# Optimization experiments

Hardware: AMD Instinct MI355X
Metric: run time of the kernel (lower is better)

Reference implementation:

```python
import jax, jax.numpy as jnp
import numpy as np

IN_FEATURES = 4096
OUT_FEATURES = 4096
K = 0.5  # keep top-k fraction of weights by |score|


def setup_inputs() -> dict:
    key = jax.random.key(0)
    kx, kw, ks = jax.random.split(key, 3)
    x = jax.random.normal(kx, (8192, IN_FEATURES), dtype=jnp.float32)
    # kaiming_normal_(mode='fan_in', nonlinearity='relu'): std = sqrt(2/fan_in)
    std = float(np.sqrt(2.0 / IN_FEATURES))
    weights = jax.random.normal(kw, (OUT_FEATURES, IN_FEATURES), dtype=jnp.float32) * std
    bias = jnp.zeros((OUT_FEATURES,), dtype=jnp.float32)
    # scores init to ones in torch, but perturb so the top-k selection is non-degenerate
    scores = jnp.ones((OUT_FEATURES, IN_FEATURES), dtype=jnp.float32) + 0.01 * jax.random.normal(ks, (OUT_FEATURES, IN_FEATURES), dtype=jnp.float32)
    return {"x": x, "weights": weights, "bias": bias, "scores": scores}


def _topk_mask(s):
    # Reproduces torch sort-based thresholding: flatten, sort ascending,
    # bottom j = int((1-K)*n) entries -> 0, remaining top entries -> 1.
    flat = s.ravel()
    n = flat.shape[0]
    j = int((1.0 - K) * n)
    order = jnp.argsort(flat)  # ascending
    keep = (jnp.arange(n) >= j).astype(s.dtype)
    mask_flat = jnp.zeros((n,), dtype=s.dtype).at[order].set(keep)
    return mask_flat.reshape(s.shape)


def reference(x, weights, bias, scores):
    s = jnp.abs(scores)
    hard = _topk_mask(s)
    # straight-through estimator: forward uses hard mask, grad passes to |scores|
    mask = s + jax.lax.stop_gradient(hard - s)
    pruned = weights * mask  # [out, in]
    return x @ pruned.T + bias  # [B, out]
```

## Files before the change

### kernel.cpp

```cpp
#include <hip/hip_runtime.h>


#define NTOT   16777216u
#define JDROP  8388608u
#define MDIM   8192
#define NDIM   4096
#define KDIM   4096

typedef __bf16 v8bf __attribute__((ext_vector_type(8)));
typedef float  v4f  __attribute__((ext_vector_type(4)));

__device__ __forceinline__ unsigned short f2bf(float f){
  unsigned u = __float_as_uint(f);
  u += 0x7fffu + ((u >> 16) & 1u);
  return (unsigned short)(u >> 16);
}

__global__ void zero_hist(unsigned* hist, unsigned* h15g){
  h15g[blockIdx.x*256 + threadIdx.x] = 0u;
  if (blockIdx.x==0) hist[threadIdx.x] = 0u;
}

__global__ __launch_bounds__(256) void hist_pass(const float* __restrict__ scores,
                                                 unsigned* __restrict__ hist,
                                                 const unsigned* __restrict__ state,
                                                 int p){
  __shared__ __align__(16) unsigned char pc[256*256];
  int tid = threadIdx.x;
  unsigned* pz = (unsigned*)pc;
  #pragma unroll
  for (int k=0;k<64;++k) pz[tid + k*256] = 0u;
  __syncthreads();
  unsigned prefix = (p>0) ? state[0] : 0u;
  const float4* s4 = (const float4*)(scores + (size_t)blockIdx.x * 16384);
  for (int it=0; it<16; ++it){
    float4 v = s4[(size_t)it*256 + tid];
    #pragma unroll
    for (int e=0;e<4;++e){
      float f = (e==0)?v.x:(e==1)?v.y:(e==2)?v.z:v.w;
      unsigned u = __float_as_uint(f) & 0x7fffffffu;
      unsigned d, ok;
      if (p==0){ d = u>>23;         ok = 1u; }
      else     { d = (u>>15)&0xffu; ok = ((u>>23)==prefix); }
      if (ok) pc[d*256 + tid]++;
    }
  }
  __syncthreads();
  unsigned b = (unsigned)tid;
  const unsigned* row = (const unsigned*)(pc + b*256);
  unsigned s = 0;
  for (int kk=0;kk<64;++kk){
    int k = (kk + tid) & 63;
    unsigned w = row[k];
    s += (w & 0xffu) + ((w>>8)&0xffu) + ((w>>16)&0xffu) + (w>>24);
  }
  if (s) atomicAdd(&hist[b], s);
}

__global__ void select_pass(unsigned* hist, unsigned* state, int p){
  int lane = threadIdx.x;
  unsigned c[4];
  #pragma unroll
  for (int k=0;k<4;++k){ c[k] = hist[lane*4+k]; hist[lane*4+k] = 0u; }
  unsigned s = c[0]+c[1]+c[2]+c[3];
  unsigned inc = s;
  #pragma unroll
  for (int d=1; d<64; d<<=1){
    unsigned t = (unsigned)__shfl_up((int)inc, d, 64);
    if (lane >= d) inc += t;
  }
  unsigned excl = inc - s;
  unsigned target = (p==0) ? JDROP : state[1];
  unsigned oldpre = (p==0) ? 0u    : state[0];
  if (target >= excl && target < excl + s){
    unsigned cum = excl, digit = 0, below = 0;
    #pragma unroll
    for (int k=0;k<4;++k){
      if (target < cum + c[k]){ digit = (unsigned)lane*4u + (unsigned)k; below = cum; break; }
      cum += c[k];
    }
    state[0] = (oldpre << 8) | digit;
    state[1] = target - below;
  }
}

__global__ __launch_bounds__(256) void hist15_pass(const float* __restrict__ scores,
                                                   const unsigned* __restrict__ state,
                                                   unsigned* __restrict__ h15g){
  __shared__ unsigned h[32768];
  int tid = threadIdx.x;
  #pragma unroll
  for (int k=0;k<128;++k) h[tid + k*256] = 0u;
  __syncthreads();
  const unsigned pre16 = state[0];
  const float4* s4 = (const float4*)(scores + (size_t)blockIdx.x * 16384);
  for (int it=0; it<16; ++it){
    float4 v = s4[(size_t)it*256 + tid];
    #pragma unroll
    for (int e=0;e<4;++e){
      float f = (e==0)?v.x:(e==1)?v.y:(e==2)?v.z:v.w;
      unsigned u = __float_as_uint(f) & 0x7fffffffu;
      if ((u>>15) == pre16) atomicAdd(&h[u & 0x7fffu], 1u);
    }
  }
  __syncthreads();
  #pragma unroll
  for (int k=0;k<128;++k){
    unsigned v = h[tid + k*256];
    if (v) atomicAdd(&h15g[tid + k*256], v);
  }
}

__global__ void select15(const unsigned* __restrict__ h15g, unsigned* state){
  int lane = threadIdx.x;
  unsigned s = 0;
  for (int k=0;k<512;++k) s += h15g[lane*512 + k];
  unsigned inc = s;
  #pragma unroll
  for (int d=1; d<64; d<<=1){
    unsigned t = (unsigned)__shfl_up((int)inc, d, 64);
    if (lane >= d) inc += t;
  }
  unsigned excl = inc - s;
  unsigned target = state[1];
  if (target >= excl && target < excl + s){
    unsigned cum = excl, digit = 0, below = 0;
    for (int k=0;k<512;++k){
      unsigned c = h15g[lane*512 + k];
      if (target < cum + c){ digit = (unsigned)(lane*512 + k); below = cum; break; }
      cum += c;
    }
    state[0] = (state[0] << 15) | digit;
    state[1] = target - below;
  }
}

__global__ __launch_bounds__(256) void tie_count(const float* __restrict__ scores,
                                                 const unsigned* __restrict__ state,
                                                 unsigned* __restrict__ tieCnt){
  unsigned T = state[0];
  int tid = threadIdx.x;
  const float4* s4 = (const float4*)(scores + (size_t)blockIdx.x * 4096);
  unsigned cnt = 0;
  for (int it=0; it<4; ++it){
    float4 v = s4[it*256 + tid];
    #pragma unroll
    for (int e=0;e<4;++e){
      float f = (e==0)?v.x:(e==1)?v.y:(e==2)?v.z:v.w;
      unsigned u = __float_as_uint(f) & 0x7fffffffu;
      cnt += (u == T) ? 1u : 0u;
    }
  }
  __shared__ unsigned r[256];
  r[tid] = cnt; __syncthreads();
  for (int s=128; s>0; s>>=1){ if (tid < s) r[tid] += r[tid+s]; __syncthreads(); }
  if (tid==0) tieCnt[blockIdx.x] = r[0];
}

__global__ __launch_bounds__(1024) void tie_scan(const unsigned* tieCnt, unsigned* tieBase){
  int tid = threadIdx.x;
  unsigned v[4], pre[4], s = 0;
  #pragma unroll
  for (int k=0;k<4;++k){ v[k] = tieCnt[tid*4+k]; pre[k] = s; s += v[k]; }
  __shared__ unsigned sc[1024];
  sc[tid] = s; __syncthreads();
  for (int d=1; d<1024; d<<=1){
    unsigned t = (tid >= d) ? sc[tid-d] : 0u;
    __syncthreads();
    sc[tid] += t;
    __syncthreads();
  }
  unsigned excl = sc[tid] - s;
  #pragma unroll
  for (int k=0;k<4;++k) tieBase[tid*4+k] = excl + pre[k];
}

__global__ __launch_bounds__(256) void build_pruned(const float* __restrict__ scores,
                                                    const float* __restrict__ w,
                                                    const unsigned* __restrict__ state,
                                                    const unsigned* __restrict__ tieBase,
                                                    unsigned short* __restrict__ wpr){
  const int row  = blockIdx.x*4 + (threadIdx.x >> 6);
  const int lane = threadIdx.x & 63;
  const unsigned T = state[0], D = state[1];
  unsigned runBase = tieBase[row];
  const float4* s4 = (const float4*)(scores + (size_t)row*4096);
  const float4* w4 = (const float4*)(w      + (size_t)row*4096);
  ushort4*      o4 = (ushort4*)(wpr + (size_t)row*4096);
  const unsigned long long below = (lane==0)?0ull:((~0ull) >> (64-lane));
  for (int it=0; it<16; ++it){
    float4 sv = s4[it*64 + lane];
    float4 wv = w4[it*64 + lane];
    unsigned u0 = __float_as_uint(sv.x) & 0x7fffffffu;
    unsigned u1 = __float_as_uint(sv.y) & 0x7fffffffu;
    unsigned u2 = __float_as_uint(sv.z) & 0x7fffffffu;
    unsigned u3 = __float_as_uint(sv.w) & 0x7fffffffu;
    bool t0=(u0==T), t1=(u1==T), t2=(u2==T), t3=(u3==T);
    unsigned long long b0=__ballot(t0), b1=__ballot(t1), b2=__ballot(t2), b3=__ballot(t3);
    unsigned lanesBelow = (unsigned)(__popcll(b0&below)+__popcll(b1&below)
                                   + __popcll(b2&below)+__popcll(b3&below));
    unsigned base = runBase + lanesBelow;
    unsigned r0 = base;
    unsigned r1 = base + (t0?1u:0u);
    unsigned r2 = r1   + (t1?1u:0u);
    unsigned r3 = r2   + (t2?1u:0u);
    bool k0 = (u0>T) || (t0 && r0>=D);
    bool k1 = (u1>T) || (t1 && r1>=D);
    bool k2 = (u2>T) || (t2 && r2>=D);
    bool k3 = (u3>T) || (t3 && r3>=D);
    ushort4 o;
    o.x = k0 ? f2bf(wv.x) : (unsigned short)0;
    o.y = k1 ? f2bf(wv.y) : (unsigned short)0;
    o.z = k2 ? f2bf(wv.z) : (unsigned short)0;
    o.w = k3 ? f2bf(wv.w) : (unsigned short)0;
    o4[it*64 + lane] = o;
    runBase += (unsigned)(__popcll(b0)+__popcll(b1)+__popcll(b2)+__popcll(b3));
  }
}

__global__ __launch_bounds__(256) void convert_x(const float4* __restrict__ x,
                                                 ushort4* __restrict__ xb){
  size_t i = (size_t)blockIdx.x * 256 + threadIdx.x;
  float4 v = x[i];
  ushort4 o; o.x=f2bf(v.x); o.y=f2bf(v.y); o.z=f2bf(v.z); o.w=f2bf(v.w);
  xb[i] = o;
}

__device__ __forceinline__ void gload_lds16b(const void* g, void* l){
  __builtin_amdgcn_global_load_lds(
      (__attribute__((address_space(1))) void*)g,
      (__attribute__((address_space(3))) void*)l, 16, 0, 0);
}

__device__ __forceinline__ void stage_mat(const unsigned short* __restrict__ G, int rowBase,
                                          unsigned short (* __restrict__ S)[64],
                                          int kt, int wid, int lane){
  #pragma unroll
  for (int hj=0; hj<4; ++hj){
    const int rg0 = (hj>>1)*128 + (wid*2 + (hj&1))*8;
    const int rg  = rg0 + (lane>>3);
    const int c16 = (lane&7) ^ (rg & 7);
    gload_lds16b(G + (size_t)(rowBase + rg)*KDIM + kt*64 + c16*8, &S[rg0][0]);
  }
}

__device__ __forceinline__ v8bf ldsfrag(const unsigned short (* __restrict__ S)[64],
                                        int row, int kc){
  return *(const v8bf*)&S[row][(kc ^ (row & 7))*8];
}

#define BAR()   { __builtin_amdgcn_s_barrier(); asm volatile("" ::: "memory"); }
#define LGKM0() asm volatile("s_waitcnt lgkmcnt(0)" ::: "memory")

__device__ __forceinline__ void ktile(const unsigned short* __restrict__ A,
                                      const unsigned short* __restrict__ B,
                                      unsigned short (* __restrict__ Asq)[64],
                                      unsigned short (* __restrict__ Bsq)[64],
                                      int Mb, int Nb, int t,
                                      int wr, int wc, int wid, int lane,
                                      v4f acc[8][4]){
  const int r16 = lane & 15, kg = lane >> 4;
  const bool pf = (t + 2 < KDIM/64);

  v8bf a0[4][2], b0[2][2];
  #pragma unroll
  for (int i=0;i<4;++i)
    #pragma unroll
    for (int ks=0;ks<2;++ks)
      a0[i][ks] = ldsfrag(Asq, wr*128 + i*16 + r16, ks*4 + kg);
  #pragma unroll
  for (int n=0;n<2;++n)
    #pragma unroll
    for (int ks=0;ks<2;++ks)
      b0[n][ks] = ldsfrag(Bsq, wc*64 + n*16 + r16, ks*4 + kg);
  BAR(); LGKM0();
  __builtin_amdgcn_s_setprio(1);
  #pragma unroll
  for (int i=0;i<4;++i)
    #pragma unroll
    for (int n=0;n<2;++n)
      #pragma unroll
      for (int ks=0;ks<2;++ks)
        acc[i][n] = __builtin_amdgcn_mfma_f32_16x16x32_bf16(a0[i][ks], b0[n][ks], acc[i][n], 0,0,0);
  __builtin_amdgcn_s_setprio(0);
  BAR();

  v8bf b1[2][2];
  #pragma unroll
  for (int n=0;n<2;++n)
    #pragma unroll
    for (int ks=0;ks<2;++ks)
      b1[n][ks] = ldsfrag(Bsq, wc*64 + (2+n)*16 + r16, ks*4 + kg);
  BAR(); LGKM0();
  __builtin_amdgcn_s_setprio(1);
  #pragma unroll
  for (int i=0;i<4;++i)
    #pragma unroll
    for (int n=0;n<2;++n)
      #pragma unroll
      for (int ks=0;ks<2;++ks)
        acc[i][2+n] = __builtin_amdgcn_mfma_f32_16x16x32_bf16(a0[i][ks], b1[n][ks], acc[i][2+n], 0,0,0);
  __builtin_amdgcn_s_setprio(0);
  BAR();

  v8bf a1[4][2];
  #pragma unroll
  for (int i=0;i<4;++i)
    #pragma unroll
    for (int ks=0;ks<2;++ks)
      a1[i][ks] = ldsfrag(Asq, wr*128 + 64 + i*16 + r16, ks*4 + kg);
  if (pf) stage_mat(B, Nb, Bsq, t+2, wid, lane);
  BAR(); LGKM0();
  __builtin_amdgcn_s_setprio(1);
  #pragma unroll
  for (int i=0;i<4;++i)
    #pragma unroll
    for (int n=0;n<2;++n)
      #pragma unroll
      for (int ks=0;ks<2;++ks)
        acc[4+i][n] = __builtin_amdgcn_mfma_f32_16x16x32_bf16(a1[i][ks], b0[n][ks], acc[4+i][n], 0,0,0);
  __builtin_amdgcn_s_setprio(0);
  BAR();

  if (pf) stage_mat(A, Mb, Asq, t+2, wid, lane);
  __builtin_amdgcn_s_setprio(1);
  #pragma unroll
  for (int i=0;i<4;++i)
    #pragma unroll
    for (int n=0;n<2;++n)
      #pragma unroll
      for (int ks=0;ks<2;++ks)
        acc[4+i][2+n] = __builtin_amdgcn_mfma_f32_16x16x32_bf16(a1[i][ks], b1[n][ks], acc[4+i][2+n], 0,0,0);
  __builtin_amdgcn_s_setprio(0);
  if (pf) { asm volatile("s_waitcnt vmcnt(8)" ::: "memory"); }
  else    { asm volatile("s_waitcnt vmcnt(0)" ::: "memory"); }
  BAR();
}

__global__ __launch_bounds__(512, 2) void gemm256(const unsigned short* __restrict__ A,
                                                  const unsigned short* __restrict__ B,
                                                  const float* __restrict__ bias,
                                                  float* __restrict__ out){
  __shared__ __align__(16) unsigned short As[2][256][64];
  __shared__ __align__(16) unsigned short Bs[2][256][64];

  const int bid = blockIdx.x;
  const int swz = (bid & 7) * 64 + (bid >> 3);
  const int Mb  = (swz >> 4) * 256;
  const int Nb  = (swz & 15) * 256;

  const int tid  = threadIdx.x;
  const int lane = tid & 63;
  const int wid  = tid >> 6;
  const int wr   = wid >> 2;
  const int wc   = wid & 3;

  v4f acc[8][4];
  #pragma unroll
  for (int i=0;i<8;++i)
    #pragma unroll
    for (int n=0;n<4;++n) acc[i][n] = (v4f){0.f,0.f,0.f,0.f};

  stage_mat(A, Mb, As[0], 0, wid, lane);
  stage_mat(B, Nb, Bs[0], 0, wid, lane);
  stage_mat(A, Mb, As[1], 1, wid, lane);
  stage_mat(B, Nb, Bs[1], 1, wid, lane);
  asm volatile("s_waitcnt vmcnt(8)" ::: "memory");
  BAR();

  #pragma unroll 1
  for (int t = 0; t < KDIM/64; t += 2){
    ktile(A, B, As[0], Bs[0], Mb, Nb, t,   wr, wc, wid, lane, acc);
    ktile(A, B, As[1], Bs[1], Mb, Nb, t+1, wr, wc, wid, lane, acc);
  }

  #pragma unroll
  for (int mt=0; mt<8; ++mt){
    const int gm0 = Mb + wr*128 + mt*16 + (lane >> 4)*4;
    #pragma unroll
    for (int nt=0; nt<4; ++nt){
      const int gn = Nb + wc*64 + nt*16 + (lane & 15);
      const float bv = bias[gn];
      v4f a = acc[mt][nt];
      #pragma unroll
      for (int r=0; r<4; ++r)
        out[(size_t)(gm0 + r)*NDIM + gn] = a[r] + bv;
    }
  }
}

extern "C" void kernel_launch(void* const* d_in, const int* in_sizes, int n_in,
                              void* d_out, int out_size, void* d_ws, size_t ws_size,
                              hipStream_t stream){
  const float* x      = (const float*)d_in[0];
  const float* w      = (const float*)d_in[1];
  const float* bias   = (const float*)d_in[2];
  const float* scores = (const float*)d_in[3];
  float* out = (float*)d_out;

  char* ws = (char*)d_ws;
  unsigned* hist    = (unsigned*)(ws);
  unsigned* state   = (unsigned*)(ws + 1024);
  unsigned* tieCnt  = (unsigned*)(ws + 2048);
  unsigned* tieBase = (unsigned*)(ws + 2048 + 16384);
  unsigned short* xb  = (unsigned short*)(ws + 65536);
  unsigned short* wpr = (unsigned short*)(ws + 65536 + (size_t)MDIM*KDIM*2);
  unsigned* h15g = (unsigned*)(ws + 65536);

  zero_hist<<<128, 256, 0, stream>>>(hist, h15g);
  for (int p = 0; p < 2; ++p){
    hist_pass<<<1024, 256, 0, stream>>>(scores, hist, state, p);
    select_pass<<<1, 64, 0, stream>>>(hist, state, p);
  }
  hist15_pass<<<1024, 256, 0, stream>>>(scores, state, h15g);
  select15<<<1, 64, 0, stream>>>(h15g, state);
  tie_count<<<4096, 256, 0, stream>>>(scores, state, tieCnt);
  tie_scan<<<1, 1024, 0, stream>>>(tieCnt, tieBase);
  build_pruned<<<1024, 256, 0, stream>>>(scores, w, state, tieBase, wpr);
  convert_x<<<MDIM*KDIM/4/256, 256, 0, stream>>>((const float4*)x, (ushort4*)xb);

  gemm256<<<dim3(512), 512, 0, stream>>>(xb, wpr, bias, out);
}
```

Measured before the change: 735.9 us.

## Fold tie scan into build_pruned, widen hist15 blocks, parallelize select15

Removes the separate single-block tie_scan kernel. Each build_pruned block now derives its row's running tie base by reducing the tieCnt entries before it, which adds redundant per-block reads in exchange for one fewer launch and serial step. hist15_pass moves from 1024 blocks of 256 threads to 256 blocks of 512 threads, so four times fewer shared histograms are flushed to the global 32K-bin histogram with atomics. select15 uses 256 threads with a shared-memory scan instead of one 64-lane wave walking 512 bins per lane, which shortens the serial selection step.

```diff
diff --git a/kernel.cpp b/kernel.cpp
--- a/kernel.cpp
+++ b/kernel.cpp
@@ -84,18 +84,19 @@
   }
 }
 
-__global__ __launch_bounds__(256) void hist15_pass(const float* __restrict__ scores,
+__global__ __launch_bounds__(512) void hist15_pass(const float* __restrict__ scores,
                                                    const unsigned* __restrict__ state,
                                                    unsigned* __restrict__ h15g){
   __shared__ unsigned h[32768];
   int tid = threadIdx.x;
   #pragma unroll
-  for (int k=0;k<128;++k) h[tid + k*256] = 0u;
+  for (int k=0;k<64;++k) h[tid + k*512] = 0u;
   __syncthreads();
   const unsigned pre16 = state[0];
-  const float4* s4 = (const float4*)(scores + (size_t)blockIdx.x * 16384);
-  for (int it=0; it<16; ++it){
-    float4 v = s4[(size_t)it*256 + tid];
+  const float4* s4 = (const float4*)scores;
+  const size_t base = (size_t)blockIdx.x * 16384;
+  for (int it=0; it<32; ++it){
+    float4 v = s4[base + (size_t)it*512 + tid];
     #pragma unroll
     for (int e=0;e<4;++e){
       float f = (e==0)?v.x:(e==1)?v.y:(e==2)?v.z:v.w;
@@ -105,29 +106,32 @@
   }
   __syncthreads();
   #pragma unroll
-  for (int k=0;k<128;++k){
-    unsigned v = h[tid + k*256];
-    if (v) atomicAdd(&h15g[tid + k*256], v);
-  }
-}
-
-__global__ void select15(const unsigned* __restrict__ h15g, unsigned* state){
-  int lane = threadIdx.x;
+  for (int k=0;k<64;++k){
+    unsigned v = h[tid + k*512];
+    if (v) atomicAdd(&h15g[tid + k*512], v);
+  }
+}
+
+__global__ __launch_bounds__(256) void select15(const unsigned* __restrict__ h15g,
+                                                unsigned* state){
+  int tid = threadIdx.x;
   unsigned s = 0;
-  for (int k=0;k<512;++k) s += h15g[lane*512 + k];
-  unsigned inc = s;
-  #pragma unroll
-  for (int d=1; d<64; d<<=1){
-    unsigned t = (unsigned)__shfl_up((int)inc, d, 64);
-    if (lane >= d) inc += t;
-  }
-  unsigned excl = inc - s;
+  for (int k=0;k<128;++k) s += h15g[tid*128 + k];
+  __shared__ unsigned sc[256];
+  sc[tid] = s; __syncthreads();
+  for (int d=1; d<256; d<<=1){
+    unsigned t = (tid >= d) ? sc[tid-d] : 0u;
+    __syncthreads();
+    sc[tid] += t;
+    __syncthreads();
+  }
+  unsigned excl = sc[tid] - s;
   unsigned target = state[1];
   if (target >= excl && target < excl + s){
     unsigned cum = excl, digit = 0, below = 0;
-    for (int k=0;k<512;++k){
-      unsigned c = h15g[lane*512 + k];
-      if (target < cum + c){ digit = (unsigned)(lane*512 + k); below = cum; break; }
+    for (int k=0;k<128;++k){
+      unsigned c = h15g[tid*128 + k];
+      if (target < cum + c){ digit = (unsigned)(tid*128 + k); below = cum; break; }
       cum += c;
     }
     state[0] = (state[0] << 15) | digit;
@@ -157,40 +161,34 @@
   if (tid==0) tieCnt[blockIdx.x] = r[0];
 }
 
-__global__ __launch_bounds__(1024) void tie_scan(const unsigned* tieCnt, unsigned* tieBase){
-  int tid = threadIdx.x;
-  unsigned v[4], pre[4], s = 0;
-  #pragma unroll
-  for (int k=0;k<4;++k){ v[k] = tieCnt[tid*4+k]; pre[k] = s; s += v[k]; }
-  __shared__ unsigned sc[1024];
-  sc[tid] = s; __syncthreads();
-  for (int d=1; d<1024; d<<=1){
-    unsigned t = (tid >= d) ? sc[tid-d] : 0u;
-    __syncthreads();
-    sc[tid] += t;
-    __syncthreads();
-  }
-  unsigned excl = sc[tid] - s;
-  #pragma unroll
-  for (int k=0;k<4;++k) tieBase[tid*4+k] = excl + pre[k];
-}
-
 __global__ __launch_bounds__(256) void build_pruned(const float* __restrict__ scores,
                                                     const float* __restrict__ w,
                                                     const unsigned* __restrict__ state,
-                                                    const unsigned* __restrict__ tieBase,
+                                                    const unsigned* __restrict__ tieCnt,
                                                     unsigned short* __restrict__ wpr){
-  const int row  = blockIdx.x*4 + (threadIdx.x >> 6);
-  const int lane = threadIdx.x & 63;
+  const int tid  = threadIdx.x;
+  const int lane = tid & 63;
+  const int wv   = tid >> 6;
+  const int rowFirst = blockIdx.x*4;
+  const int row  = rowFirst + wv;
+
+  unsigned part = 0;
+  for (int j = tid; j < rowFirst; j += 256) part += tieCnt[j];
+  __shared__ unsigned red[256];
+  red[tid] = part; __syncthreads();
+  for (int s=128; s>0; s>>=1){ if (tid < s) red[tid] += red[tid+s]; __syncthreads(); }
+  unsigned runBase = red[0];
+  #pragma unroll
+  for (int i=0;i<3;++i) if (i < wv) runBase += tieCnt[rowFirst + i];
+
   const unsigned T = state[0], D = state[1];
-  unsigned runBase = tieBase[row];
   const float4* s4 = (const float4*)(scores + (size_t)row*4096);
   const float4* w4 = (const float4*)(w      + (size_t)row*4096);
   ushort4*      o4 = (ushort4*)(wpr + (size_t)row*4096);
   const unsigned long long below = (lane==0)?0ull:((~0ull) >> (64-lane));
   for (int it=0; it<16; ++it){
     float4 sv = s4[it*64 + lane];
-    float4 wv = w4[it*64 + lane];
+    float4 wvv = w4[it*64 + lane];
     unsigned u0 = __float_as_uint(sv.x) & 0x7fffffffu;
     unsigned u1 = __float_as_uint(sv.y) & 0x7fffffffu;
     unsigned u2 = __float_as_uint(sv.z) & 0x7fffffffu;
@@ -209,10 +207,10 @@
     bool k2 = (u2>T) || (t2 && r2>=D);
     bool k3 = (u3>T) || (t3 && r3>=D);
     ushort4 o;
-    o.x = k0 ? f2bf(wv.x) : (unsigned short)0;
-    o.y = k1 ? f2bf(wv.y) : (unsigned short)0;
-    o.z = k2 ? f2bf(wv.z) : (unsigned short)0;
-    o.w = k3 ? f2bf(wv.w) : (unsigned short)0;
+    o.x = k0 ? f2bf(wvv.x) : (unsigned short)0;
+    o.y = k1 ? f2bf(wvv.y) : (unsigned short)0;
+    o.z = k2 ? f2bf(wvv.z) : (unsigned short)0;
+    o.w = k3 ? f2bf(wvv.w) : (unsigned short)0;
     o4[it*64 + lane] = o;
     runBase += (unsigned)(__popcll(b0)+__popcll(b1)+__popcll(b2)+__popcll(b3));
   }
@@ -402,7 +400,6 @@
   unsigned* hist    = (unsigned*)(ws);
   unsigned* state   = (unsigned*)(ws + 1024);
   unsigned* tieCnt  = (unsigned*)(ws + 2048);
-  unsigned* tieBase = (unsigned*)(ws + 2048 + 16384);
   unsigned short* xb  = (unsigned short*)(ws + 65536);
   unsigned short* wpr = (unsigned short*)(ws + 65536 + (size_t)MDIM*KDIM*2);
   unsigned* h15g = (unsigned*)(ws + 65536);
@@ -412,11 +409,10 @@
     hist_pass<<<1024, 256, 0, stream>>>(scores, hist, state, p);
     select_pass<<<1, 64, 0, stream>>>(hist, state, p);
   }
-  hist15_pass<<<1024, 256, 0, stream>>>(scores, state, h15g);
-  select15<<<1, 64, 0, stream>>>(h15g, state);
+  hist15_pass<<<256, 512, 0, stream>>>(scores, state, h15g);
+  select15<<<1, 256, 0, stream>>>(h15g, state);
   tie_count<<<4096, 256, 0, stream>>>(scores, state, tieCnt);
-  tie_scan<<<1, 1024, 0, stream>>>(tieCnt, tieBase);
-  build_pruned<<<1024, 256, 0, stream>>>(scores, w, state, tieBase, wpr);
+  build_pruned<<<1024, 256, 0, stream>>>(scores, w, state, tieCnt, wpr);
   convert_x<<<MDIM*KDIM/4/256, 256, 0, stream>>>((const float4*)x, (ushort4*)xb);
 
   gemm256<<<dim3(512), 512, 0, stream>>>(xb, wpr, bias, out);
```

After: 682.0 us. 7.3% less time.
